# Kernel optimization log

Measured on AMD Instinct MI355X. Metric: run time of the kernel, lower is better.

## Reference

```python
import jax, jax.numpy as jnp
import numpy as np

B, T, D = 4, 1024, 1024
H = 16                      # attention heads
DS, DC, EXP = 16, 4, 2      # d_state, d_conv, expand
DIN = EXP * D               # 2048
DTR = D // 16               # dt_rank = 64
TOPK_RATIO = 0.25
EPS = 1e-5


def setup_inputs() -> dict:
    key = jax.random.key(0)
    ks = jax.random.split(key, 16)
    def n(k, shape, scale=0.02):
        return jax.random.normal(k, shape, jnp.float32) * scale
    return {
        "x": jax.random.normal(ks[0], (B, T, D), jnp.float32),
        "ln_w": jnp.ones((D,), jnp.float32),
        "ln_b": jnp.zeros((D,), jnp.float32),
        "r_w1": n(ks[1], (D, D // 2)),
        "r_b1": jnp.zeros((D // 2,), jnp.float32),
        "r_w2": n(ks[2], (D // 2, 1)),
        "r_b2": jnp.zeros((1,), jnp.float32),
        "Wq": n(ks[3], (D, D)), "bq": jnp.zeros((D,), jnp.float32),
        "Wk": n(ks[4], (D, D)), "bk": jnp.zeros((D,), jnp.float32),
        "Wv": n(ks[5], (D, D)), "bv": jnp.zeros((D,), jnp.float32),
        "Wo": n(ks[6], (D, D)), "bo": jnp.zeros((D,), jnp.float32),
        "in_w": n(ks[7], (D, 2 * DIN)),
        "conv_w": n(ks[8], (DIN, DC), 0.1),
        "conv_b": jnp.zeros((DIN,), jnp.float32),
        "xproj_w": n(ks[9], (DIN, DTR + 2 * DS)),
        "dt_w": n(ks[10], (DTR, DIN), 0.1),
        "dt_b": jnp.full((DIN,), -4.0, jnp.float32) + n(ks[11], (DIN,), 0.1),
        "A_log": jnp.log(jnp.broadcast_to(jnp.arange(1, DS + 1, dtype=jnp.float32), (DIN, DS))),
        "Dp": jnp.ones((DIN,), jnp.float32),
        "out_w": n(ks[12], (DIN, D)),
    }


def _attn_core(x, Wq, bq, Wk, bk, Wv, bv, Wo, bo):
    b, L, d = x.shape
    hd = d // H
    q = (x @ Wq + bq).reshape(b, L, H, hd)
    k = (x @ Wk + bk).reshape(b, L, H, hd)
    v = (x @ Wv + bv).reshape(b, L, H, hd)
    scores = jnp.einsum('bqhd,bkhd->bhqk', q, k) / jnp.sqrt(jnp.float32(hd))
    p = jax.nn.softmax(scores, axis=-1)
    o = jnp.einsum('bhqk,bkhd->bqhd', p, v).reshape(b, L, d)
    return o @ Wo + bo


def _ssm_core(u, in_w, conv_w, conv_b, xproj_w, dt_w, dt_b, A_log, Dp, out_w):
    # Mamba-style selective SSM on the sub-sequence u: (b, L, D)
    b, L, _ = u.shape
    xi, z = jnp.split(u @ in_w, 2, axis=-1)            # (b, L, DIN) each
    xp = jnp.pad(xi, ((0, 0), (DC - 1, 0), (0, 0)))    # causal depthwise conv1d
    xc = conv_b + sum(xp[:, j:j + L] * conv_w[:, j] for j in range(DC))
    xc = jax.nn.silu(xc)
    proj = xc @ xproj_w                                # (b, L, DTR + 2*DS)
    dtp = proj[..., :DTR]
    Bm = proj[..., DTR:DTR + DS]
    Cm = proj[..., DTR + DS:]
    delta = jax.nn.softplus(dtp @ dt_w + dt_b)         # (b, L, DIN)
    A = -jnp.exp(A_log)                                # (DIN, DS)
    dA = jnp.exp(delta[..., None] * A)                 # (b, L, DIN, DS)
    dBu = (delta * xc)[..., None] * Bm[:, :, None, :]  # (b, L, DIN, DS)

    def step(h, inp):
        dA_t, dBu_t, C_t = inp
        h = dA_t * h + dBu_t                           # (b, DIN, DS)
        return h, jnp.einsum('bds,bs->bd', h, C_t)

    xs = (jnp.moveaxis(dA, 1, 0), jnp.moveaxis(dBu, 1, 0), jnp.moveaxis(Cm, 1, 0))
    _, ys = jax.lax.scan(step, jnp.zeros((b, DIN, DS), u.dtype), xs)
    y = jnp.moveaxis(ys, 0, 1) + xc * Dp               # (b, L, DIN)
    y = y * jax.nn.silu(z)
    return y @ out_w


def reference(x, ln_w, ln_b, r_w1, r_b1, r_w2, r_b2, Wq, bq, Wk, bk, Wv, bv, Wo, bo,
              in_w, conv_w, conv_b, xproj_w, dt_w, dt_b, A_log, Dp, out_w):
    b, t, d = x.shape
    k = min(max(1, int(TOPK_RATIO * t)), t)            # static top-k count
    # pre-norm (LayerNorm)
    mu = x.mean(-1, keepdims=True)
    var = ((x - mu) ** 2).mean(-1, keepdims=True)
    xn = (x - mu) * jax.lax.rsqrt(var + EPS) * ln_w + ln_b
    # router scores (b, t) and top-k dispatch
    scores = jnp.squeeze(jax.nn.gelu(xn @ r_w1 + r_b1) @ r_w2 + r_b2, -1)
    _, topk_idx = jax.lax.top_k(scores, k)
    bidx = jnp.arange(b)[:, None]
    mask = jnp.zeros((b, t), bool).at[bidx, topk_idx].set(True)
    # unselected positions in ascending order (stable sort of 0/1 mask)
    order = jnp.argsort(mask.astype(jnp.int32), axis=1)
    bottom_idx = order[:, :t - k]
    # SSM branch on bottom (t-k) tokens, order-preserving
    x_ssm = xn[bidx, bottom_idx]                       # (b, t-k, d)
    d_ssm_tok = _ssm_core(x_ssm, in_w, conv_w, conv_b, xproj_w, dt_w, dt_b, A_log, Dp, out_w)
    delta_ssm = jnp.zeros_like(xn).at[bidx, bottom_idx].set(d_ssm_tok)
    # attention branch on top-k tokens only (sparse attention)
    x_attn = xn[bidx, topk_idx]                        # (b, k, d)
    d_attn_tok = _attn_core(x_attn, Wq, bq, Wk, bk, Wv, bv, Wo, bo)
    delta_attn = jnp.zeros_like(xn).at[bidx, topk_idx].set(d_attn_tok)
    # masked merge + residual
    delta = jnp.where(mask[..., None], delta_attn, delta_ssm)
    return x + delta
```

## Files before the change

### kernel.cpp

```cpp
#include <hip/hip_runtime.h>
#include <hip/hip_bf16.h>
#include <cstdint>
#include <cstddef>

typedef unsigned short u16;
typedef __attribute__((ext_vector_type(8))) short short8;
typedef __attribute__((ext_vector_type(4))) float f32x4;

__device__ __forceinline__ float b2f(u16 h){ union{unsigned u; float f;} c; c.u = ((unsigned)h)<<16; return c.f; }
__device__ __forceinline__ u16 f2b(float f){ union{float f; unsigned u;} c; c.f = f; unsigned u = c.u; return (u16)((u + 0x7fffu + ((u>>16)&1u)) >> 16); }
__device__ __forceinline__ float gelu_f(float x){
  float x3 = x*x*x;
  return 0.5f*x*(1.f + tanhf(0.7978845608028654f*(x + 0.044715f*x3)));
}
__device__ __forceinline__ void gload_lds16(const void* g, void* l){
  __builtin_amdgcn_global_load_lds((const __attribute__((address_space(1))) void*)g,
                                   (__attribute__((address_space(3))) void*)l, 16, 0, 0);
}

__global__ __launch_bounds__(256) void k_ln(const float* __restrict__ x, const float* __restrict__ w,
    const float* __restrict__ b, float* __restrict__ xn)
{
  int t = blockIdx.x, tid = threadIdx.x;
  float4 v = ((const float4*)(x + (size_t)t*1024))[tid];
  float s = v.x+v.y+v.z+v.w;
  #pragma unroll
  for (int o=32;o;o>>=1) s += __shfl_xor(s,o,64);
  __shared__ float r1[4], r2[4];
  if ((tid&63)==0) r1[tid>>6] = s;
  __syncthreads();
  float mu = (r1[0]+r1[1]+r1[2]+r1[3]) * (1.f/1024.f);
  float4 c = {v.x-mu, v.y-mu, v.z-mu, v.w-mu};
  float q = c.x*c.x+c.y*c.y+c.z*c.z+c.w*c.w;
  #pragma unroll
  for (int o=32;o;o>>=1) q += __shfl_xor(q,o,64);
  if ((tid&63)==0) r2[tid>>6] = q;
  __syncthreads();
  float inv = rsqrtf((r2[0]+r2[1]+r2[2]+r2[3])*(1.f/1024.f) + 1e-5f);
  float4 wv = ((const float4*)w)[tid];
  float4 bv = ((const float4*)b)[tid];
  float4 o4 = {c.x*inv*wv.x+bv.x, c.y*inv*wv.y+bv.y, c.z*inv*wv.z+bv.z, c.w*inv*wv.w+bv.w};
  ((float4*)(xn + (size_t)t*1024))[tid] = o4;
}

__global__ __launch_bounds__(256) void k_tcvt(const float* __restrict__ src, u16* __restrict__ dst, int R, int C)
{
  __shared__ float tile[32][33];
  int c0 = blockIdx.x*32, r0 = blockIdx.y*32;
  int lc = threadIdx.x & 31, lr = threadIdx.x >> 5;
  #pragma unroll
  for (int rr=0; rr<4; rr++) tile[lr + rr*8][lc] = src[(size_t)(r0 + lr + rr*8)*C + c0 + lc];
  __syncthreads();
  #pragma unroll
  for (int rr=0; rr<4; rr++) dst[(size_t)(c0 + lr + rr*8)*R + r0 + lc] = f2b(tile[lc][lr + rr*8]);
}

__global__ __launch_bounds__(256) void k_bpack(const float* __restrict__ bq, const float* __restrict__ bk,
    const float* __restrict__ bv, float* __restrict__ o)
{
  int i = blockIdx.x*256 + threadIdx.x;
  o[i] = (i < 1024) ? bq[i] : ((i < 2048) ? bk[i-1024] : bv[i-2048]);
}

__global__ __launch_bounds__(256) void k_splitA(const float* __restrict__ xn, u16* __restrict__ ap)
{
  int t = blockIdx.x;
  int k4 = threadIdx.x*4;
  float4 v = *(const float4*)&xn[(size_t)t*1024 + k4];
  union{u16 u[4]; uint2 d;} hi, lo;
  float xs[4] = {v.x, v.y, v.z, v.w};
  #pragma unroll
  for (int e=0;e<4;e++){ u16 h = f2b(xs[e]); hi.u[e]=h; lo.u[e]=f2b(xs[e]-b2f(h)); }
  u16* row = ap + (size_t)t*3072;
  *(uint2*)&row[k4]      = hi.d;
  *(uint2*)&row[1024+k4] = hi.d;
  *(uint2*)&row[2048+k4] = lo.d;
}

__global__ __launch_bounds__(256) void k_splitB(const float* __restrict__ w1, u16* __restrict__ bp)
{
  __shared__ float tile[32][33];
  int n0 = blockIdx.x*32, k0 = blockIdx.y*32;
  int lc = threadIdx.x & 31, lr = threadIdx.x >> 5;
  #pragma unroll
  for (int rr=0; rr<4; rr++) tile[lr+rr*8][lc] = w1[(size_t)(k0+lr+rr*8)*512 + n0+lc];
  __syncthreads();
  #pragma unroll
  for (int rr=0; rr<4; rr++){
    int n = n0 + lr + rr*8, k = k0 + lc;
    float x = tile[lc][lr+rr*8];
    u16 hi = f2b(x);
    u16 lo = f2b(x - b2f(hi));
    u16* row = bp + (size_t)n*3072;
    row[k] = hi; row[1024+k] = lo; row[2048+k] = hi;
  }
}

__global__ __launch_bounds__(256) void k_score3(const float* __restrict__ ps, const float* __restrict__ b2,
    float* __restrict__ scores)
{
  int i = blockIdx.x*256 + threadIdx.x;
  float s = b2[0];
  #pragma unroll
  for (int p=0;p<16;p++) s += ps[p*4096 + i];
  scores[i] = s;
}

__global__ __launch_bounds__(1024) void k_topk(const float* __restrict__ scores, int* __restrict__ aidx, int* __restrict__ sidx)
{
  int b = blockIdx.x, tid = threadIdx.x;
  __shared__ float s[1024];
  __shared__ int pf[1024];
  s[tid] = scores[b*1024 + tid];
  __syncthreads();
  float my = s[tid];
  int cnt = 0;
  for (int j=0;j<1024;j++){ float sj = s[j]; cnt += (sj > my) || (sj == my && j < tid); }
  int isa = (cnt < 256) ? 1 : 0;
  pf[tid] = isa; __syncthreads();
  for (int o=1;o<1024;o<<=1){
    int add = (tid >= o) ? pf[tid-o] : 0;
    __syncthreads();
    pf[tid] += add;
    __syncthreads();
  }
  int excl = pf[tid] - isa;
  if (isa) aidx[b*256 + excl] = tid;
  else     sidx[b*768 + (tid - excl)] = tid;
}

__global__ __launch_bounds__(256) void k_gather(const float* __restrict__ xn, const int* __restrict__ aidx,
    const int* __restrict__ sidx, u16* __restrict__ xat, u16* __restrict__ xst)
{
  int id = blockIdx.x;
  int b = id >> 10, s = id & 1023;
  int src; u16* dst;
  if (s < 256) { src = aidx[b*256 + s]; dst = xat + (size_t)(b*256 + s)*1024; }
  else { int ss = s - 256; src = sidx[b*768 + ss]; dst = xst + (size_t)(b*768 + ss)*1024; }
  const float4* sp = (const float4*)(xn + ((size_t)b*1024 + src)*1024);
  int tid = threadIdx.x;
  float4 vv = sp[tid];
  union { u16 u[4]; uint2 d; } pk;
  pk.u[0]=f2b(vv.x); pk.u[1]=f2b(vv.y); pk.u[2]=f2b(vv.z); pk.u[3]=f2b(vv.w);
  ((uint2*)dst)[tid] = pk.d;
}

template<int BM, int BN>
__global__ __launch_bounds__(256) void k_mfma(const u16* __restrict__ A, int lda,
    const u16* __restrict__ Bt, int ldb, const float* __restrict__ bias,
    float* __restrict__ outf, u16* __restrict__ outb, int M, int N, int K,
    int act, int split)
{
  constexpr int WTM = BM/2, WTN = BN/2;
  constexpr int MI = WTM/16, NJ = WTN/16;
  __shared__ u16 lA[2][BM*32];
  __shared__ u16 lB[2][BN*32];
  const int tid = threadIdx.x;
  const int lane = tid & 63;
  const int wv = tid >> 6;
  const int wm = wv >> 1, wn = wv & 1;
  const int tm = blockIdx.x * BM, tn = blockIdx.y * BN;
  const int r0 = lane & 15;
  const int kg = lane >> 4;

  const int ksl = K / gridDim.z;
  const int kbeg = blockIdx.z * ksl;
  if (gridDim.z > 1) outf += (size_t)blockIdx.z * ((size_t)M * N);

  auto stage = [&](int buf, int kt){
    for (int c = tid; c < BM*4; c += 256) {
      int row = c >> 2, j = c & 3;
      int jj = j ^ ((row >> 1) & 3);
      gload_lds16(&A[(size_t)(tm + row)*lda + kt + jj*8], &lA[buf][c*8]);
    }
    for (int c = tid; c < BN*4; c += 256) {
      int row = c >> 2, j = c & 3;
      int jj = j ^ ((row >> 1) & 3);
      gload_lds16(&Bt[(size_t)(tn + row)*ldb + kt + jj*8], &lB[buf][c*8]);
    }
  };

  f32x4 acc[MI][NJ];
  #pragma unroll
  for (int i=0;i<MI;i++)
    #pragma unroll
    for (int j=0;j<NJ;j++) acc[i][j] = (f32x4){0.f,0.f,0.f,0.f};

  stage(0, kbeg);
  __syncthreads();
  const int nk = ksl / 32;
  int cur = 0;
  for (int t = 0; t < nk; t++) {
    if (t + 1 < nk) stage(cur ^ 1, kbeg + (t+1)*32);
    short8 av[MI], bvv[NJ];
    #pragma unroll
    for (int i=0;i<MI;i++){
      int row = wm*WTM + i*16 + r0;
      av[i] = *(const short8*)&lA[cur][row*32 + ((kg ^ ((row>>1)&3))<<3)];
    }
    #pragma unroll
    for (int j=0;j<NJ;j++){
      int row = wn*WTN + j*16 + r0;
      bvv[j] = *(const short8*)&lB[cur][row*32 + ((kg ^ ((row>>1)&3))<<3)];
    }
    #pragma unroll
    for (int i=0;i<MI;i++)
      #pragma unroll
      for (int j=0;j<NJ;j++)
        acc[i][j] = __builtin_amdgcn_mfma_f32_16x16x32_bf16(av[i], bvv[j], acc[i][j], 0, 0, 0);
    __syncthreads();
    cur ^= 1;
  }

  if (act == 3) {
    const float* w2 = (const float*)outb;
    #pragma unroll
    for (int i=0;i<MI;i++){
      #pragma unroll
      for (int r=0;r<4;r++){
        float t = 0.f;
        #pragma unroll
        for (int j=0;j<NJ;j++){
          int col = tn + wn*WTN + j*16 + r0;
          t += gelu_f(acc[i][j][r] + bias[col]) * w2[col];
        }
        #pragma unroll
        for (int o=1;o<16;o<<=1) t += __shfl_xor(t, o, 64);
        if (r0 == 0)
          outf[(size_t)(blockIdx.y*2 + wn)*M + tm + wm*WTM + i*16 + kg*4 + r] = t;
      }
    }
    return;
  }

  const int rr = kg * 4;
  #pragma unroll
  for (int i=0;i<MI;i++){
    #pragma unroll
    for (int j=0;j<NJ;j++){
      #pragma unroll
      for (int r=0;r<4;r++){
        int row = tm + wm*WTM + i*16 + rr + r;
        int col = tn + wn*WTN + j*16 + r0;
        float v = acc[i][j][r];
        if (bias) v += bias[col];
        if (act == 1) v = (v > 15.f) ? v : log1pf(__expf(v));
        else if (act == 2) v = gelu_f(v);
        if (col < split) outf[(size_t)row*split + col] = v;
        else             outb[(size_t)row*(N-split) + (col-split)] = f2b(v);
      }
    }
  }
}

__global__ __launch_bounds__(256) void k_psum(const float* __restrict__ p, float* __restrict__ o,
    u16* __restrict__ dtpb)
{
  int i = blockIdx.x*256 + threadIdx.x;
  float v = p[i] + p[i+294912] + p[i+589824] + p[i+884736];
  o[i] = v;
  int tok = i / 96, col = i - tok*96;
  if (col < 64) dtpb[tok*64 + col] = f2b(v);
}

__global__ __launch_bounds__(256) void k_attn2(const u16* __restrict__ qkv, u16* __restrict__ ob)
{
  __shared__ u16 lKP[16384];
  __shared__ u16 lVt[16384];
  char* KP = (char*)lKP;
  char* VT = (char*)lVt;
  const int tid = threadIdx.x;
  const int lane = tid & 63;
  const int w = tid >> 6;
  const int bx = blockIdx.x;
  const int b = bx >> 6, h = (bx >> 2) & 15, ch = bx & 3;

  const u16* kbase = qkv + (size_t)(b*256)*3072 + 1024 + h*64;
  const u16* vbase = qkv + (size_t)(b*256)*3072 + 2048 + h*64;

  {
    int rr = tid >> 3;
    int c8 = (tid & 7) * 8;
    for (int i = 0; i < 8; i++) {
      int row = i*32 + rr;
      int4 kv = *(const int4*)&kbase[(size_t)row*3072 + c8];
      int koff = row*128 + c8*2;
      *(int4*)(KP + (koff ^ ((row & 7) << 4))) = kv;
      int4 vv = *(const int4*)&vbase[(size_t)row*3072 + c8];
      union { int4 q; u16 u[8]; } vu; vu.q = vv;
      #pragma unroll
      for (int jj = 0; jj < 8; jj++) {
        int j = (jj + rr) & 7;
        int d = c8 + j;
        int voff = d*512 + row*2;
        *(u16*)(VT + (voff ^ ((d & 7) << 4))) = vu.u[j];
      }
    }
  }

  const int r0 = lane & 15;
  const int kg = lane >> 4;
  const int qrow = ch*64 + w*16 + r0;
  const u16* qp = qkv + (size_t)(b*256 + qrow)*3072 + h*64 + kg*8;
  short8 qf0 = *(const short8*)(qp);
  short8 qf1 = *(const short8*)(qp + 32);

  __syncthreads();

  f32x4 acc[16];
  #pragma unroll
  for (int t = 0; t < 16; t++) acc[t] = (f32x4){0.f,0.f,0.f,0.f};
  #pragma unroll
  for (int t = 0; t < 16; t++) {
    int row = t*16 + r0;
    int base = row*128 + kg*16;
    short8 kf0 = *(const short8*)(KP + ((base     ) ^ ((row & 7) << 4)));
    short8 kf1 = *(const short8*)(KP + ((base + 64) ^ ((row & 7) << 4)));
    acc[t] = __builtin_amdgcn_mfma_f32_16x16x32_bf16(qf0, kf0, acc[t], 0, 0, 0);
    acc[t] = __builtin_amdgcn_mfma_f32_16x16x32_bf16(qf1, kf1, acc[t], 0, 0, 0);
  }

  #pragma unroll
  for (int t = 0; t < 16; t++) acc[t] = acc[t] * 0.125f;
  float lsum[4];
  #pragma unroll
  for (int r = 0; r < 4; r++) {
    float mx = -1e30f;
    #pragma unroll
    for (int t = 0; t < 16; t++) mx = fmaxf(mx, acc[t][r]);
    #pragma unroll
    for (int o = 1; o < 16; o <<= 1) mx = fmaxf(mx, __shfl_xor(mx, o, 64));
    float s = 0.f;
    #pragma unroll
    for (int t = 0; t < 16; t++) { float p = __expf(acc[t][r] - mx); acc[t][r] = p; s += p; }
    #pragma unroll
    for (int o = 1; o < 16; o <<= 1) s += __shfl_xor(s, o, 64);
    lsum[r] = s;
  }

  __syncthreads();
  char* PW = KP + w*8192;
  #pragma unroll
  for (int t = 0; t < 16; t++) {
    int col = t*16 + r0;
    #pragma unroll
    for (int r = 0; r < 4; r++) {
      int row = kg*4 + r;
      int off = row*512 + col*2;
      *(u16*)(PW + (off ^ ((row & 7) << 4))) = f2b(acc[t][r]);
    }
  }

  f32x4 oacc[4];
  #pragma unroll
  for (int dt = 0; dt < 4; dt++) oacc[dt] = (f32x4){0.f,0.f,0.f,0.f};
  #pragma unroll
  for (int kc = 0; kc < 8; kc++) {
    int pbase = r0*512 + kc*64 + kg*16;
    short8 pf = *(const short8*)(PW + (pbase ^ ((r0 & 7) << 4)));
    #pragma unroll
    for (int dt = 0; dt < 4; dt++) {
      int vrow = dt*16 + r0;
      int vb2 = vrow*512 + kc*64 + kg*16;
      short8 vf = *(const short8*)(VT + (vb2 ^ ((vrow & 7) << 4)));
      oacc[dt] = __builtin_amdgcn_mfma_f32_16x16x32_bf16(pf, vf, oacc[dt], 0, 0, 0);
    }
  }

  u16* op = ob + (size_t)(b*256 + ch*64 + w*16)*1024 + h*64;
  #pragma unroll
  for (int dt = 0; dt < 4; dt++) {
    #pragma unroll
    for (int r = 0; r < 4; r++) {
      int row = kg*4 + r;
      float v = oacc[dt][r] / lsum[r];
      op[(size_t)row*1024 + dt*16 + r0] = f2b(v);
    }
  }
}

__global__ __launch_bounds__(256) void k_conv(const float* __restrict__ xi, const float* __restrict__ cw,
    const float* __restrict__ cb, float* __restrict__ xc, u16* __restrict__ xcb)
{
  size_t idx = (size_t)blockIdx.x*256 + threadIdx.x;
  int d = (int)(idx & 2047);
  size_t bt = idx >> 11;
  int t = (int)(bt % 768);
  float acc = cb[d];
  const float* p = xi + idx;
  float w0=cw[d*4+0], w1=cw[d*4+1], w2=cw[d*4+2], w3=cw[d*4+3];
  acc += w3 * p[0];
  if (t >= 1) acc += w2 * p[-2048];
  if (t >= 2) acc += w1 * p[-4096];
  if (t >= 3) acc += w0 * p[-6144];
  float sv = acc / (1.f + __expf(-acc));
  xc[idx]  = sv;
  xcb[idx] = f2b(sv);
}

__global__ __launch_bounds__(256) void k_scan1(const float* __restrict__ delta, const float* __restrict__ xc,
    const float* __restrict__ proj, const float* __restrict__ A_log, float* __restrict__ cs)
{
  int bid = blockIdx.x;
  int db = bid & 7;
  int c  = (bid >> 3) & 15;
  int b  = bid >> 7;
  int d  = db*256 + threadIdx.x;
  float Ar[16];
  #pragma unroll
  for (int s=0;s<16;s++) Ar[s] = -__expf(A_log[d*16+s]);
  float ap[16], hc[16];
  #pragma unroll
  for (int s=0;s<16;s++){ ap[s]=1.f; hc[s]=0.f; }
  size_t row0 = (size_t)b*768 + c*48;
  for (int t=0;t<48;t++){
    size_t row = row0 + t;
    float dl = delta[row*2048 + d];
    float xv = xc[row*2048 + d];
    float du = dl*xv;
    const float4* bp = (const float4*)&proj[row*96 + 64];
    float4 b0 = bp[0], b1 = bp[1], b2 = bp[2], b3 = bp[3];
    float Bc[16] = {b0.x,b0.y,b0.z,b0.w,b1.x,b1.y,b1.z,b1.w,
                    b2.x,b2.y,b2.z,b2.w,b3.x,b3.y,b3.z,b3.w};
    #pragma unroll
    for (int s=0;s<16;s++){
      float dA = __expf(dl*Ar[s]);
      ap[s] *= dA;
      hc[s] = dA*hc[s] + du*Bc[s];
    }
  }
  size_t base = ((size_t)(b*16 + c)*32)*2048 + d;
  #pragma unroll
  for (int s=0;s<16;s++){
    cs[base + (size_t)s*2048]      = ap[s];
    cs[base + (size_t)(16+s)*2048] = hc[s];
  }
}

__global__ __launch_bounds__(256) void k_scan2(float* __restrict__ cs)
{
  int bid = blockIdx.x;
  int db = bid & 7;
  int s  = (bid >> 3) & 15;
  int b  = bid >> 7;
  int d  = db*256 + threadIdx.x;
  float h = 0.f;
  for (int c=0;c<16;c++){
    size_t base = ((size_t)(b*16 + c)*32)*2048 + d;
    float ap = cs[base + (size_t)s*2048];
    float hc = cs[base + (size_t)(16+s)*2048];
    cs[base + (size_t)(16+s)*2048] = h;
    h = ap*h + hc;
  }
}

__global__ __launch_bounds__(256) void k_scan3(const float* __restrict__ delta, const float* __restrict__ xc,
    const float* __restrict__ proj, const float* __restrict__ cs, const u16* __restrict__ zb,
    const float* __restrict__ A_log, const float* __restrict__ Dp, u16* __restrict__ yb)
{
  int bid = blockIdx.x;
  int db = bid & 7;
  int c  = (bid >> 3) & 15;
  int b  = bid >> 7;
  int d  = db*256 + threadIdx.x;
  float Ar[16];
  #pragma unroll
  for (int s=0;s<16;s++) Ar[s] = -__expf(A_log[d*16+s]);
  float dpv = Dp[d];
  float h[16];
  size_t base = ((size_t)(b*16 + c)*32)*2048 + d;
  #pragma unroll
  for (int s=0;s<16;s++) h[s] = cs[base + (size_t)(16+s)*2048];
  size_t row0 = (size_t)b*768 + c*48;
  for (int t=0;t<48;t++){
    size_t row = row0 + t;
    float dl = delta[row*2048 + d];
    float xv = xc[row*2048 + d];
    float du = dl*xv;
    const float4* bp = (const float4*)&proj[row*96 + 64];
    float4 b0 = bp[0], b1 = bp[1], b2 = bp[2], b3 = bp[3];
    const float4* cp = (const float4*)&proj[row*96 + 80];
    float4 c0 = cp[0], c1 = cp[1], c2 = cp[2], c3 = cp[3];
    float Bc[16] = {b0.x,b0.y,b0.z,b0.w,b1.x,b1.y,b1.z,b1.w,
                    b2.x,b2.y,b2.z,b2.w,b3.x,b3.y,b3.z,b3.w};
    float Cc[16] = {c0.x,c0.y,c0.z,c0.w,c1.x,c1.y,c1.z,c1.w,
                    c2.x,c2.y,c2.z,c2.w,c3.x,c3.y,c3.z,c3.w};
    float y = 0.f;
    #pragma unroll
    for (int s=0;s<16;s++){
      float dA = __expf(dl*Ar[s]);
      h[s] = dA*h[s] + du*Bc[s];
      y += h[s]*Cc[s];
    }
    y += xv*dpv;
    float z = b2f(zb[row*2048 + d]);
    float g = z / (1.f + __expf(-z));
    yb[row*2048 + d] = f2b(y*g);
  }
}

__global__ __launch_bounds__(256) void k_scat(const float* __restrict__ x, const int* __restrict__ idxarr,
    const float* __restrict__ dlt, float* __restrict__ out, int per_b)
{
  int id = blockIdx.x;
  int b = id / per_b;
  int t = idxarr[id];
  const float4* xp = (const float4*)(x + ((size_t)b*1024 + t)*1024);
  const float4* dp = (const float4*)(dlt + (size_t)id*1024);
  float4* op = (float4*)(out + ((size_t)b*1024 + t)*1024);
  int tid = threadIdx.x;
  float4 a = xp[tid], d = dp[tid];
  op[tid] = (float4){a.x+d.x, a.y+d.y, a.z+d.z, a.w+d.w};
}

extern "C" void kernel_launch(void* const* d_in, const int* in_sizes, int n_in,
                              void* d_out, int out_size, void* d_ws, size_t ws_size,
                              hipStream_t stream)
{
  const float* x      = (const float*)d_in[0];
  const float* ln_w   = (const float*)d_in[1];
  const float* ln_b   = (const float*)d_in[2];
  const float* r_w1   = (const float*)d_in[3];
  const float* r_b1   = (const float*)d_in[4];
  const float* r_w2   = (const float*)d_in[5];
  const float* r_b2   = (const float*)d_in[6];
  const float* Wq     = (const float*)d_in[7];
  const float* bq     = (const float*)d_in[8];
  const float* Wk     = (const float*)d_in[9];
  const float* bk     = (const float*)d_in[10];
  const float* Wv     = (const float*)d_in[11];
  const float* bv     = (const float*)d_in[12];
  const float* Wo     = (const float*)d_in[13];
  const float* bo     = (const float*)d_in[14];
  const float* in_w   = (const float*)d_in[15];
  const float* conv_w = (const float*)d_in[16];
  const float* conv_b = (const float*)d_in[17];
  const float* xproj_w= (const float*)d_in[18];
  const float* dt_w   = (const float*)d_in[19];
  const float* dt_b   = (const float*)d_in[20];
  const float* A_log  = (const float*)d_in[21];
  const float* Dp     = (const float*)d_in[22];
  const float* out_w  = (const float*)d_in[23];
  float* out = (float*)d_out;

  uint8_t* ws = (uint8_t*)d_ws;
  size_t off = 0;
  auto alloc = [&](size_t bytes)->uint8_t*{
    uint8_t* p = ws + off;
    off += (bytes + 255) & ~(size_t)255;
    return p;
  };

  float* xn    = (float*)alloc(4096ull*1024*4);
  u16*   wqt   = (u16*)  alloc(1024ull*1024*2);
  u16*   wkt   = (u16*)  alloc(1024ull*1024*2);
  u16*   wvt   = (u16*)  alloc(1024ull*1024*2);
  u16*   wot   = (u16*)  alloc(1024ull*1024*2);
  u16*   inwt  = (u16*)  alloc(4096ull*1024*2);
  u16*   outwt = (u16*)  alloc(1024ull*2048*2);
  u16*   xpwt  = (u16*)  alloc(96ull*2048*2);
  u16*   dtwt  = (u16*)  alloc(2048ull*64*2);
  u16*   r1pk  = (u16*)  alloc(512ull*3072*2);
  float* scores= (float*)alloc(4096*4);
  int*   aidx  = (int*)  alloc(1024*4);
  int*   sidx  = (int*)  alloc(3072*4);
  u16*   xat   = (u16*)  alloc(1024ull*1024*2);
  u16*   xst   = (u16*)  alloc(3072ull*1024*2);
  float* qkvb  = (float*)alloc(3072*4);

  float* s_projp = xn;
  float* cs = xn;

  uint8_t* arena = ws + off;
  u16*   apk = (u16*)(arena);
  float* ps  = (float*)(arena + 25165824);
  u16*   qkvbuf = (u16*)(arena);
  u16*   obuf   = (u16*)(arena + 6291456);
  float* adelta = (float*)(arena + 8388608);
  float* s_xi   = (float*)(arena);
  u16*   s_zb   = (u16*)(arena + 25165824);
  float* s_xc   = (float*)(arena + 37748736);
  u16*   s_xcb  = (u16*)(arena + 62914560);
  float* s_proj = (float*)(arena + 75497472);
  u16*   s_dtpb = (u16*)(arena + 76677120);
  float* s_delta  = s_xi;
  u16*   s_yb     = s_xcb;
  float* s_sdelta = (float*)s_zb;

  hipLaunchKernelGGL(k_ln, dim3(4096), dim3(256), 0, stream, x, ln_w, ln_b, xn);
  hipLaunchKernelGGL(k_tcvt, dim3(32,32),  dim3(256), 0, stream, Wq,     wqt,   1024, 1024);
  hipLaunchKernelGGL(k_tcvt, dim3(32,32),  dim3(256), 0, stream, Wk,     wkt,   1024, 1024);
  hipLaunchKernelGGL(k_tcvt, dim3(32,32),  dim3(256), 0, stream, Wv,     wvt,   1024, 1024);
  hipLaunchKernelGGL(k_tcvt, dim3(32,32),  dim3(256), 0, stream, Wo,     wot,   1024, 1024);
  hipLaunchKernelGGL(k_tcvt, dim3(128,32), dim3(256), 0, stream, in_w,   inwt,  1024, 4096);
  hipLaunchKernelGGL(k_tcvt, dim3(32,64),  dim3(256), 0, stream, out_w,  outwt, 2048, 1024);
  hipLaunchKernelGGL(k_tcvt, dim3(3,64),   dim3(256), 0, stream, xproj_w,xpwt,  2048, 96);
  hipLaunchKernelGGL(k_tcvt, dim3(64,2),   dim3(256), 0, stream, dt_w,   dtwt,  64,   2048);
  hipLaunchKernelGGL(k_bpack, dim3(12), dim3(256), 0, stream, bq, bk, bv, qkvb);
  hipLaunchKernelGGL(k_splitB, dim3(16,32), dim3(256), 0, stream, r_w1, r1pk);
  hipLaunchKernelGGL(k_splitA, dim3(4096), dim3(256), 0, stream, xn, apk);
  hipLaunchKernelGGL((k_mfma<64,64>), dim3(64,8), dim3(256), 0, stream,
      apk, 3072, r1pk, 3072, r_b1, ps, (u16*)r_w2, 4096, 512, 3072, 3, 0);
  hipLaunchKernelGGL(k_score3, dim3(16), dim3(256), 0, stream, ps, r_b2, scores);
  hipLaunchKernelGGL(k_topk, dim3(4), dim3(1024), 0, stream, scores, aidx, sidx);
  hipLaunchKernelGGL(k_gather, dim3(4096), dim3(256), 0, stream, xn, aidx, sidx, xat, xst);
  hipLaunchKernelGGL((k_mfma<32,128>), dim3(32,24), dim3(256), 0, stream,
      xat, 1024, wqt, 1024, qkvb, (float*)nullptr, qkvbuf, 1024, 3072, 1024, 0, 0);
  hipLaunchKernelGGL(k_attn2, dim3(256), dim3(256), 0, stream, qkvbuf, obuf);
  hipLaunchKernelGGL((k_mfma<32,64>), dim3(32,16), dim3(256), 0, stream,
      obuf, 1024, wot, 1024, bo, adelta, (u16*)nullptr, 1024, 1024, 1024, 0, 1024);
  hipLaunchKernelGGL(k_scat, dim3(1024), dim3(256), 0, stream, x, aidx, adelta, out, 256);
  hipLaunchKernelGGL((k_mfma<128,128>), dim3(24,32), dim3(256), 0, stream,
      xst, 1024, inwt, 1024, (const float*)nullptr, s_xi, s_zb, 3072, 4096, 1024, 0, 2048);
  hipLaunchKernelGGL(k_conv, dim3(24576), dim3(256), 0, stream, s_xi, conv_w, conv_b, s_xc, s_xcb);
  hipLaunchKernelGGL((k_mfma<32,96>), dim3(96,1,4), dim3(256), 0, stream,
      s_xcb, 2048, xpwt, 2048, (const float*)nullptr, s_projp, (u16*)nullptr, 3072, 96, 2048, 0, 96);
  hipLaunchKernelGGL(k_psum, dim3(1152), dim3(256), 0, stream, s_projp, s_proj, s_dtpb);
  hipLaunchKernelGGL((k_mfma<64,128>), dim3(48,16), dim3(256), 0, stream,
      s_dtpb, 64, dtwt, 64, dt_b, s_delta, (u16*)nullptr, 3072, 2048, 64, 1, 2048);
  hipLaunchKernelGGL(k_scan1, dim3(512), dim3(256), 0, stream, s_delta, s_xc, s_proj, A_log, cs);
  hipLaunchKernelGGL(k_scan2, dim3(512), dim3(256), 0, stream, cs);
  hipLaunchKernelGGL(k_scan3, dim3(512), dim3(256), 0, stream, s_delta, s_xc, s_proj, cs, s_zb, A_log, Dp, s_yb);
  hipLaunchKernelGGL((k_mfma<32,128>), dim3(96,8), dim3(256), 0, stream,
      s_yb, 2048, outwt, 2048, (const float*)nullptr, s_sdelta, (u16*)nullptr, 3072, 1024, 2048, 0, 1024);
  hipLaunchKernelGGL(k_scat, dim3(3072), dim3(256), 0, stream, x, sidx, s_sdelta, out, 768);
}
```

Measured before the change: 436.0 us.

## Fuse split into layernorm, remap blocks across XCDs, use bf16 SSM scan inputs

Folds the hi/lo bf16 split of the normalized input into the layernorm kernel, removing one launch and one re-read of xn. The GEMM kernel remaps workgroup IDs so that neighbouring tiles land on the same XCD, which should improve L2 reuse. The conv output is now stored only as bf16, and the dt projection writes delta in bf16. The scan kernels read these bf16 buffers, halving that traffic at the cost of some precision in the recurrence inputs.

Result: slower. 448.4 us (+2.8%).

```diff
diff --git a/kernel.cpp b/kernel.cpp
--- a/kernel.cpp
+++ b/kernel.cpp
@@ -19,7 +19,7 @@
 }
 
 __global__ __launch_bounds__(256) void k_ln(const float* __restrict__ x, const float* __restrict__ w,
-    const float* __restrict__ b, float* __restrict__ xn)
+    const float* __restrict__ b, float* __restrict__ xn, u16* __restrict__ apk)
 {
   int t = blockIdx.x, tid = threadIdx.x;
   float4 v = ((const float4*)(x + (size_t)t*1024))[tid];
@@ -41,6 +41,15 @@
   float4 bv = ((const float4*)b)[tid];
   float4 o4 = {c.x*inv*wv.x+bv.x, c.y*inv*wv.y+bv.y, c.z*inv*wv.z+bv.z, c.w*inv*wv.w+bv.w};
   ((float4*)(xn + (size_t)t*1024))[tid] = o4;
+  union{u16 u[4]; uint2 d;} hi, lo;
+  float xs[4] = {o4.x, o4.y, o4.z, o4.w};
+  #pragma unroll
+  for (int e=0;e<4;e++){ u16 h = f2b(xs[e]); hi.u[e]=h; lo.u[e]=f2b(xs[e]-b2f(h)); }
+  u16* row = apk + (size_t)t*3072;
+  int k4 = tid*4;
+  *(uint2*)&row[k4]      = hi.d;
+  *(uint2*)&row[1024+k4] = hi.d;
+  *(uint2*)&row[2048+k4] = lo.d;
 }
 
 __global__ __launch_bounds__(256) void k_tcvt(const float* __restrict__ src, u16* __restrict__ dst, int R, int C)
@@ -60,21 +69,6 @@
 {
   int i = blockIdx.x*256 + threadIdx.x;
   o[i] = (i < 1024) ? bq[i] : ((i < 2048) ? bk[i-1024] : bv[i-2048]);
-}
-
-__global__ __launch_bounds__(256) void k_splitA(const float* __restrict__ xn, u16* __restrict__ ap)
-{
-  int t = blockIdx.x;
-  int k4 = threadIdx.x*4;
-  float4 v = *(const float4*)&xn[(size_t)t*1024 + k4];
-  union{u16 u[4]; uint2 d;} hi, lo;
-  float xs[4] = {v.x, v.y, v.z, v.w};
-  #pragma unroll
-  for (int e=0;e<4;e++){ u16 h = f2b(xs[e]); hi.u[e]=h; lo.u[e]=f2b(xs[e]-b2f(h)); }
-  u16* row = ap + (size_t)t*3072;
-  *(uint2*)&row[k4]      = hi.d;
-  *(uint2*)&row[1024+k4] = hi.d;
-  *(uint2*)&row[2048+k4] = lo.d;
 }
 
 __global__ __launch_bounds__(256) void k_splitB(const float* __restrict__ w1, u16* __restrict__ bp)
@@ -159,9 +153,21 @@
   const int lane = tid & 63;
   const int wv = tid >> 6;
   const int wm = wv >> 1, wn = wv & 1;
-  const int tm = blockIdx.x * BM, tn = blockIdx.y * BN;
   const int r0 = lane & 15;
   const int kg = lane >> 4;
+
+  int bx = blockIdx.x, by = blockIdx.y;
+  if (gridDim.z == 1) {
+    int nwg = gridDim.x * gridDim.y;
+    int f = by * gridDim.x + bx;
+    int q = nwg >> 3, r = nwg & 7;
+    int xcd = f & 7, ord = f >> 3;
+    int base = (xcd < r) ? xcd*(q+1) : r*(q+1) + (xcd - r)*q;
+    int lin = base + ord;
+    bx = lin % gridDim.x;
+    by = lin / gridDim.x;
+  }
+  const int tm = bx * BM, tn = by * BN;
 
   const int ksl = K / gridDim.z;
   const int kbeg = blockIdx.z * ksl;
@@ -227,7 +233,7 @@
         #pragma unroll
         for (int o=1;o<16;o<<=1) t += __shfl_xor(t, o, 64);
         if (r0 == 0)
-          outf[(size_t)(blockIdx.y*2 + wn)*M + tm + wm*WTM + i*16 + kg*4 + r] = t;
+          outf[(size_t)(by*2 + wn)*M + tm + wm*WTM + i*16 + kg*4 + r] = t;
       }
     }
     return;
@@ -380,7 +386,7 @@
 }
 
 __global__ __launch_bounds__(256) void k_conv(const float* __restrict__ xi, const float* __restrict__ cw,
-    const float* __restrict__ cb, float* __restrict__ xc, u16* __restrict__ xcb)
+    const float* __restrict__ cb, u16* __restrict__ xcb)
 {
   size_t idx = (size_t)blockIdx.x*256 + threadIdx.x;
   int d = (int)(idx & 2047);
@@ -394,11 +400,10 @@
   if (t >= 2) acc += w1 * p[-4096];
   if (t >= 3) acc += w0 * p[-6144];
   float sv = acc / (1.f + __expf(-acc));
-  xc[idx]  = sv;
   xcb[idx] = f2b(sv);
 }
 
-__global__ __launch_bounds__(256) void k_scan1(const float* __restrict__ delta, const float* __restrict__ xc,
+__global__ __launch_bounds__(256) void k_scan1(const u16* __restrict__ delta, const u16* __restrict__ xcb,
     const float* __restrict__ proj, const float* __restrict__ A_log, float* __restrict__ cs)
 {
   int bid = blockIdx.x;
@@ -415,8 +420,8 @@
   size_t row0 = (size_t)b*768 + c*48;
   for (int t=0;t<48;t++){
     size_t row = row0 + t;
-    float dl = delta[row*2048 + d];
-    float xv = xc[row*2048 + d];
+    float dl = b2f(delta[row*2048 + d]);
+    float xv = b2f(xcb[row*2048 + d]);
     float du = dl*xv;
     const float4* bp = (const float4*)&proj[row*96 + 64];
     float4 b0 = bp[0], b1 = bp[1], b2 = bp[2], b3 = bp[3];
@@ -454,7 +459,7 @@
   }
 }
 
-__global__ __launch_bounds__(256) void k_scan3(const float* __restrict__ delta, const float* __restrict__ xc,
+__global__ __launch_bounds__(256) void k_scan3(const u16* __restrict__ delta, const u16* __restrict__ xcb,
     const float* __restrict__ proj, const float* __restrict__ cs, const u16* __restrict__ zb,
     const float* __restrict__ A_log, const float* __restrict__ Dp, u16* __restrict__ yb)
 {
@@ -474,8 +479,8 @@
   size_t row0 = (size_t)b*768 + c*48;
   for (int t=0;t<48;t++){
     size_t row = row0 + t;
-    float dl = delta[row*2048 + d];
-    float xv = xc[row*2048 + d];
+    float dl = b2f(delta[row*2048 + d]);
+    float xv = b2f(xcb[row*2048 + d]);
     float du = dl*xv;
     const float4* bp = (const float4*)&proj[row*96 + 64];
     float4 b0 = bp[0], b1 = bp[1], b2 = bp[2], b3 = bp[3];
@@ -579,15 +584,14 @@
   float* adelta = (float*)(arena + 8388608);
   float* s_xi   = (float*)(arena);
   u16*   s_zb   = (u16*)(arena + 25165824);
-  float* s_xc   = (float*)(arena + 37748736);
   u16*   s_xcb  = (u16*)(arena + 62914560);
   float* s_proj = (float*)(arena + 75497472);
   u16*   s_dtpb = (u16*)(arena + 76677120);
-  float* s_delta  = s_xi;
+  u16*   s_deltab = (u16*)s_xi;
   u16*   s_yb     = s_xcb;
   float* s_sdelta = (float*)s_zb;
 
-  hipLaunchKernelGGL(k_ln, dim3(4096), dim3(256), 0, stream, x, ln_w, ln_b, xn);
+  hipLaunchKernelGGL(k_ln, dim3(4096), dim3(256), 0, stream, x, ln_w, ln_b, xn, apk);
   hipLaunchKernelGGL(k_tcvt, dim3(32,32),  dim3(256), 0, stream, Wq,     wqt,   1024, 1024);
   hipLaunchKernelGGL(k_tcvt, dim3(32,32),  dim3(256), 0, stream, Wk,     wkt,   1024, 1024);
   hipLaunchKernelGGL(k_tcvt, dim3(32,32),  dim3(256), 0, stream, Wv,     wvt,   1024, 1024);
@@ -598,7 +602,6 @@
   hipLaunchKernelGGL(k_tcvt, dim3(64,2),   dim3(256), 0, stream, dt_w,   dtwt,  64,   2048);
   hipLaunchKernelGGL(k_bpack, dim3(12), dim3(256), 0, stream, bq, bk, bv, qkvb);
   hipLaunchKernelGGL(k_splitB, dim3(16,32), dim3(256), 0, stream, r_w1, r1pk);
-  hipLaunchKernelGGL(k_splitA, dim3(4096), dim3(256), 0, stream, xn, apk);
   hipLaunchKernelGGL((k_mfma<64,64>), dim3(64,8), dim3(256), 0, stream,
       apk, 3072, r1pk, 3072, r_b1, ps, (u16*)r_w2, 4096, 512, 3072, 3, 0);
   hipLaunchKernelGGL(k_score3, dim3(16), dim3(256), 0, stream, ps, r_b2, scores);
@@ -612,15 +615,15 @@
   hipLaunchKernelGGL(k_scat, dim3(1024), dim3(256), 0, stream, x, aidx, adelta, out, 256);
   hipLaunchKernelGGL((k_mfma<128,128>), dim3(24,32), dim3(256), 0, stream,
       xst, 1024, inwt, 1024, (const float*)nullptr, s_xi, s_zb, 3072, 4096, 1024, 0, 2048);
-  hipLaunchKernelGGL(k_conv, dim3(24576), dim3(256), 0, stream, s_xi, conv_w, conv_b, s_xc, s_xcb);
+  hipLaunchKernelGGL(k_conv, dim3(24576), dim3(256), 0, stream, s_xi, conv_w, conv_b, s_xcb);
   hipLaunchKernelGGL((k_mfma<32,96>), dim3(96,1,4), dim3(256), 0, stream,
       s_xcb, 2048, xpwt, 2048, (const float*)nullptr, s_projp, (u16*)nullptr, 3072, 96, 2048, 0, 96);
   hipLaunchKernelGGL(k_psum, dim3(1152), dim3(256), 0, stream, s_projp, s_proj, s_dtpb);
   hipLaunchKernelGGL((k_mfma<64,128>), dim3(48,16), dim3(256), 0, stream,
-      s_dtpb, 64, dtwt, 64, dt_b, s_delta, (u16*)nullptr, 3072, 2048, 64, 1, 2048);
-  hipLaunchKernelGGL(k_scan1, dim3(512), dim3(256), 0, stream, s_delta, s_xc, s_proj, A_log, cs);
+      s_dtpb, 64, dtwt, 64, dt_b, (float*)nullptr, s_deltab, 3072, 2048, 64, 1, 0);
+  hipLaunchKernelGGL(k_scan1, dim3(512), dim3(256), 0, stream, s_deltab, s_xcb, s_proj, A_log, cs);
   hipLaunchKernelGGL(k_scan2, dim3(512), dim3(256), 0, stream, cs);
-  hipLaunchKernelGGL(k_scan3, dim3(512), dim3(256), 0, stream, s_delta, s_xc, s_proj, cs, s_zb, A_log, Dp, s_yb);
+  hipLaunchKernelGGL(k_scan3, dim3(512), dim3(256), 0, stream, s_deltab, s_xcb, s_proj, cs, s_zb, A_log, Dp, s_yb);
   hipLaunchKernelGGL((k_mfma<32,128>), dim3(96,8), dim3(256), 0, stream,
       s_yb, 2048, outwt, 2048, (const float*)nullptr, s_sdelta, (u16*)nullptr, 3072, 1024, 2048, 0, 1024);
   hipLaunchKernelGGL(k_scat, dim3(3072), dim3(256), 0, stream, x, sidx, s_sdelta, out, 768);
```
